# Performance work log

Measured on AMD Instinct MI355X. Metric: run time of the kernel, lower is better.

The kernel has to match this reference:

```python
import jax, jax.numpy as jnp
import numpy as np
import math

D_MODEL = 1024
N_HEADS = 16
B, T = 4, 2048


def setup_inputs() -> dict:
    key = jax.random.key(0)
    ks = jax.random.split(key, 10)
    s = 1.0 / math.sqrt(D_MODEL)
    x = jax.random.normal(ks[0], (B, T, D_MODEL), dtype=jnp.float32)
    # causal mask, broadcastable over batch and heads; 0 -> masked
    mask = jnp.tril(jnp.ones((T, T), dtype=jnp.int32))[None, None, :, :]
    w_q = jax.random.normal(ks[1], (D_MODEL, D_MODEL), dtype=jnp.float32) * s
    b_q = jnp.zeros((D_MODEL,), dtype=jnp.float32)
    w_k = jax.random.normal(ks[2], (D_MODEL, D_MODEL), dtype=jnp.float32) * s
    b_k = jnp.zeros((D_MODEL,), dtype=jnp.float32)
    w_v = jax.random.normal(ks[3], (D_MODEL, D_MODEL), dtype=jnp.float32) * s
    b_v = jnp.zeros((D_MODEL,), dtype=jnp.float32)
    w_o = jax.random.normal(ks[4], (D_MODEL, D_MODEL), dtype=jnp.float32) * s
    b_o = jnp.zeros((D_MODEL,), dtype=jnp.float32)
    return {"x": x, "mask": mask, "w_q": w_q, "b_q": b_q, "w_k": w_k,
            "b_k": b_k, "w_v": w_v, "b_v": b_v, "w_o": w_o, "b_o": b_o}


def reference(x, mask, w_q, b_q, w_k, b_k, w_v, b_v, w_o, b_o):
    Bx, Tx, C = x.shape
    H = N_HEADS
    d_k = C // H
    def split_heads(y):  # [B,T,C] -> [B,H,T,d_k]
        return y.reshape(Bx, Tx, H, d_k).transpose(0, 2, 1, 3)
    Q = split_heads(x @ w_q + b_q)
    K = split_heads(x @ w_k + b_k)
    V = split_heads(x @ w_v + b_v)
    scores = jnp.einsum('bhqd,bhkd->bhqk', Q, K) / math.sqrt(d_k)
    scores = jnp.where(mask == 0, jnp.float32(-1e9), scores)
    attn = jax.nn.softmax(scores, axis=-1)
    out = jnp.einsum('bhqk,bhkd->bhqd', attn, V)
    out = out.transpose(0, 2, 1, 3).reshape(Bx, Tx, C)
    return out @ w_o + b_o
```

## Files before the change

kernel.cpp:

```cpp
#include <hip/hip_runtime.h>
#include <stdint.h>

#define D_MODEL 1024
#define NH      16
#define BB      4
#define TT      2048
#define MROWS   (BB * TT)

typedef __attribute__((ext_vector_type(8))) short bf16x8;
typedef __attribute__((ext_vector_type(4))) float f32x4;

__device__ __forceinline__ unsigned short f2bf(float f) {
    union { float f; unsigned int u; } v; v.f = f;
    unsigned int r = v.u + 0x7fffu + ((v.u >> 16) & 1u);
    return (unsigned short)(r >> 16);
}

__device__ __forceinline__ unsigned short f2bf_fast(float f) {
    union { float f; unsigned int u; } v; v.f = f;
    return (unsigned short)((v.u + 0x8000u) >> 16);
}

__device__ __forceinline__ void gload_lds16(const unsigned short* g, unsigned short* l) {
    __builtin_amdgcn_global_load_lds(
        (const __attribute__((address_space(1))) void*)g,
        (__attribute__((address_space(3))) void*)l,
        16, 0, 0);
}

__global__ void convert_x_kernel(const float* __restrict__ x, unsigned short* __restrict__ xb) {
    int i = blockIdx.x * 256 + threadIdx.x;
    float4 v = ((const float4*)x)[i];
    ushort4 o;
    o.x = f2bf(v.x); o.y = f2bf(v.y); o.z = f2bf(v.z); o.w = f2bf(v.w);
    ((ushort4*)xb)[i] = o;
}

__global__ void transpose_w_kernel(const float* __restrict__ wq, const float* __restrict__ wk,
                                   const float* __restrict__ wv, const float* __restrict__ wo,
                                   unsigned short* tq, unsigned short* tk,
                                   unsigned short* tv, unsigned short* to_) {
    const float* src; unsigned short* dst;
    switch (blockIdx.z) {
        case 0:  src = wq; dst = tq; break;
        case 1:  src = wk; dst = tk; break;
        case 2:  src = wv; dst = tv; break;
        default: src = wo; dst = to_; break;
    }
    __shared__ float tile[32][33];
    int tx = threadIdx.x & 31, ty = threadIdx.x >> 5;
    int k0 = blockIdx.y * 32, n0 = blockIdx.x * 32;
    #pragma unroll
    for (int i = 0; i < 4; ++i)
        tile[ty + i * 8][tx] = src[(k0 + ty + i * 8) * D_MODEL + n0 + tx];
    __syncthreads();
    #pragma unroll
    for (int i = 0; i < 4; ++i)
        dst[(n0 + ty + i * 8) * D_MODEL + k0 + tx] = f2bf(tile[tx][ty + i * 8]);
}

__device__ __forceinline__ void gemm_mainloop(const unsigned short* __restrict__ A,
                                              const unsigned short* __restrict__ Bt,
                                              int m0, int n0,
                                              unsigned short* As, unsigned short* Bs,
                                              f32x4 acc[4][4]) {
    const int tid = threadIdx.x;
    const int lane = tid & 63, wave = tid >> 6;
    const int wm = (wave >> 1) * 64, wn = (wave & 1) * 64;
    const int l15 = lane & 15, quad = lane >> 4;
    const int rx7 = l15 & 7;
    const int srow = tid >> 3;
    const int scol = ((tid & 7) ^ (srow & 7)) * 8;
    const unsigned short* Ag = A + (size_t)(m0 + srow) * D_MODEL + scol;
    const unsigned short* Bg = Bt + (size_t)(n0 + srow) * D_MODEL + scol;
    unsigned short* AsW = As + wave * 512;
    unsigned short* BsW = Bs + wave * 512;
    for (int k0 = 0; k0 < D_MODEL; k0 += 64) {
        __syncthreads();
        #pragma unroll
        for (int p = 0; p < 4; ++p) {
            gload_lds16(Ag + k0 + (size_t)(32 * p) * D_MODEL, AsW + (32 * p) * 64);
            gload_lds16(Bg + k0 + (size_t)(32 * p) * D_MODEL, BsW + (32 * p) * 64);
        }
        __syncthreads();
        #pragma unroll
        for (int kk = 0; kk < 2; ++kk) {
            const int co = ((kk * 4 + quad) ^ rx7) * 8;
            bf16x8 af[4], bfr[4];
            #pragma unroll
            for (int mt = 0; mt < 4; ++mt)
                af[mt] = *(const bf16x8*)(As + (wm + mt * 16 + l15) * 64 + co);
            #pragma unroll
            for (int nt = 0; nt < 4; ++nt)
                bfr[nt] = *(const bf16x8*)(Bs + (wn + nt * 16 + l15) * 64 + co);
            #pragma unroll
            for (int mt = 0; mt < 4; ++mt)
                #pragma unroll
                for (int nt = 0; nt < 4; ++nt)
                    acc[mt][nt] = __builtin_amdgcn_mfma_f32_16x16x32_bf16(af[mt], bfr[nt], acc[mt][nt], 0, 0, 0);
        }
    }
}

__global__ __launch_bounds__(256, 2) void gemm_qkv_kernel(
        const unsigned short* __restrict__ Xb, const unsigned short* __restrict__ Wt,
        const float* __restrict__ bq, const float* __restrict__ bk, const float* __restrict__ bv,
        unsigned short* __restrict__ Qo, unsigned short* __restrict__ Ko,
        unsigned short* __restrict__ VTo) {
    __shared__ unsigned short S[18432];
    unsigned short* As = S;
    unsigned short* Bs = S + 8192;
    int m0 = blockIdx.y * 128, n0 = blockIdx.x * 128;
    f32x4 acc[4][4];
    #pragma unroll
    for (int mt = 0; mt < 4; ++mt)
        #pragma unroll
        for (int nt = 0; nt < 4; ++nt)
            acc[mt][nt] = (f32x4){0.f, 0.f, 0.f, 0.f};
    gemm_mainloop(Xb, Wt, m0, n0, As, Bs, acc);

    const int sel = n0 >> 10;
    const float* bias = (sel == 0) ? bq : (sel == 1) ? bk : bv;
    const float scale = (sel == 0) ? 0.125f * 1.44269504f : 1.f;
    const int tid = threadIdx.x, lane = tid & 63, wave = tid >> 6;
    const int wm = (wave >> 1) * 64, wn = (wave & 1) * 64, l15 = lane & 15, quad = lane >> 4;
    if (sel < 2) {
        unsigned short* Out = (sel == 0) ? Qo : Ko;
        __syncthreads();
        unsigned short* R = S + (wn >> 6) * 9216;
        #pragma unroll
        for (int nt = 0; nt < 4; ++nt) {
            int ln = nt * 16 + l15;
            int col = (n0 + wn + nt * 16 + l15) & 1023;
            float bv_ = bias[col];
            #pragma unroll
            for (int mt = 0; mt < 4; ++mt)
                #pragma unroll
                for (int r = 0; r < 4; ++r) {
                    int lm = wm + mt * 16 + quad * 4 + r;
                    R[lm * 72 + ln] = f2bf((acc[mt][nt][r] + bv_) * scale);
                }
        }
        __syncthreads();
        int hh = tid >> 7, t = tid & 127;
        int h0 = (n0 & 1023) >> 6;
        int b = m0 >> 11, tb = m0 & 2047;
        unsigned short* gp = Out + (size_t)((b * NH + h0 + hh) * TT + tb + t) * 64;
        const unsigned short* lp = S + hh * 9216 + t * 72;
        #pragma unroll
        for (int j = 0; j < 8; ++j)
            *(uint4*)(gp + j * 8) = *(const uint4*)(lp + j * 8);
    } else {
        #pragma unroll
        for (int nt = 0; nt < 4; ++nt) {
            int col = (n0 + wn + nt * 16 + l15) & 1023;
            float bv_ = bias[col];
            int h = col >> 6, dd = col & 63;
            #pragma unroll
            for (int mt = 0; mt < 4; ++mt) {
                int gm0 = m0 + wm + mt * 16 + quad * 4;
                int b = gm0 >> 11, t0 = gm0 & 2047;
                ushort4 o;
                o.x = f2bf(acc[mt][nt][0] + bv_);
                o.y = f2bf(acc[mt][nt][1] + bv_);
                o.z = f2bf(acc[mt][nt][2] + bv_);
                o.w = f2bf(acc[mt][nt][3] + bv_);
                *(ushort4*)&VTo[(((size_t)(b * NH + h) * 16 + (t0 >> 7)) * 64 + dd) * 128 + (t0 & 127)] = o;
            }
        }
    }
}

__global__ __launch_bounds__(256, 2) void gemm_out_kernel(
        const unsigned short* __restrict__ Ob, const unsigned short* __restrict__ Wto,
        const float* __restrict__ bo, float* __restrict__ out) {
    __shared__ unsigned short As[128 * 64], Bs[128 * 64];
    int m0 = blockIdx.y * 128, n0 = blockIdx.x * 128;
    f32x4 acc[4][4];
    #pragma unroll
    for (int mt = 0; mt < 4; ++mt)
        #pragma unroll
        for (int nt = 0; nt < 4; ++nt)
            acc[mt][nt] = (f32x4){0.f, 0.f, 0.f, 0.f};
    gemm_mainloop(Ob, Wto, m0, n0, As, Bs, acc);
    const int tid = threadIdx.x, lane = tid & 63, wave = tid >> 6;
    const int wm = (wave >> 1) * 64, wn = (wave & 1) * 64, l15 = lane & 15, quad = lane >> 4;
    #pragma unroll
    for (int nt = 0; nt < 4; ++nt) {
        int gn = n0 + wn + nt * 16 + l15;
        float bv_ = bo[gn];
        #pragma unroll
        for (int mt = 0; mt < 4; ++mt) {
            #pragma unroll
            for (int r = 0; r < 4; ++r) {
                int gm = m0 + wm + mt * 16 + quad * 4 + r;
                out[(size_t)gm * D_MODEL + gn] = acc[mt][nt][r] + bv_;
            }
        }
    }
}

__global__ __launch_bounds__(256, 2) void flash_kernel(
        const unsigned short* __restrict__ Q, const unsigned short* __restrict__ K,
        const unsigned short* __restrict__ VT, unsigned short* __restrict__ O) {
    __shared__ unsigned short Kd[2][8192];
    __shared__ unsigned short Vd[2][8192];
    __shared__ unsigned short Ps[5120];
    const int n = blockIdx.x;
    const int bh = n & 63;
    const int qt = 15 - (n >> 6);
    const int q0 = qt * 128;
    const int tid = threadIdx.x, lane = tid & 63, wave = tid >> 6;
    const int l15 = lane & 15, quad = lane >> 4;
    const int mbase = wave * 32;
    const unsigned short* Qb = Q + (size_t)bh * (TT * 64) + (size_t)q0 * 64;
    const unsigned short* Kb = K + (size_t)bh * (TT * 64);
    const unsigned short* Vtb = VT + (size_t)bh * (16 * 8192);
    unsigned short* Pw = Ps + wave * 1280;

    int koff[4], voff[4];
    #pragma unroll
    for (int p = 0; p < 4; ++p) {
        int c = p * 256 + wave * 64 + lane;
        int kr = c >> 3, ks = c & 7;
        koff[p] = kr * 64 + ((ks ^ (kr & 7)) * 8);
        int vd = c >> 4, vs = c & 15;
        voff[p] = vd * 128 + ((vs ^ (vd & 15)) * 8);
    }
    auto fire = [&](int kt, int buf) {
        const unsigned short* Ksrc = Kb + kt * 8192;
        const unsigned short* Vsrc = Vtb + kt * 8192;
        #pragma unroll
        for (int p = 0; p < 4; ++p) {
            gload_lds16(Ksrc + koff[p], &Kd[buf][(p * 256 + wave * 64) * 8]);
            gload_lds16(Vsrc + voff[p], &Vd[buf][(p * 256 + wave * 64) * 8]);
        }
    };

    bf16x8 qf[2][2];
    #pragma unroll
    for (int mt = 0; mt < 2; ++mt)
        #pragma unroll
        for (int kk = 0; kk < 2; ++kk)
            qf[mt][kk] = *(const bf16x8*)(Qb + (size_t)(mbase + mt * 16 + l15) * 64 + kk * 32 + quad * 8);

    float l_part[2][4];
    f32x4 acc[2][4];
    #pragma unroll
    for (int mt = 0; mt < 2; ++mt) {
        #pragma unroll
        for (int r = 0; r < 4; ++r) l_part[mt][r] = 0.f;
        #pragma unroll
        for (int nt = 0; nt < 4; ++nt) acc[mt][nt] = (f32x4){0.f, 0.f, 0.f, 0.f};
    }

    fire(0, 0);

    for (int kt = 0; kt <= qt; ++kt) {
        const int p = kt & 1;
        __syncthreads();
        if (kt < qt) fire(kt + 1, p ^ 1);
        const unsigned short* Ksl = Kd[p];
        const unsigned short* Vsl = Vd[p];

        #pragma unroll 1
        for (int s4 = 0; s4 < 4; ++s4) {
            f32x4 sf[2][2];
            #pragma unroll
            for (int mt = 0; mt < 2; ++mt)
                #pragma unroll
                for (int ntl = 0; ntl < 2; ++ntl) sf[mt][ntl] = (f32x4){0.f, 0.f, 0.f, 0.f};
            #pragma unroll
            for (int kk = 0; kk < 2; ++kk)
                #pragma unroll
                for (int ntl = 0; ntl < 2; ++ntl) {
                    int row = s4 * 32 + ntl * 16 + l15;
                    bf16x8 kf = *(const bf16x8*)&Ksl[row * 64 + (((kk * 4 + quad) ^ (row & 7)) * 8)];
                    #pragma unroll
                    for (int mt = 0; mt < 2; ++mt)
                        sf[mt][ntl] = __builtin_amdgcn_mfma_f32_16x16x32_bf16(qf[mt][kk], kf, sf[mt][ntl], 0, 0, 0);
                }
            if (kt == qt) {
                #pragma unroll
                for (int mt = 0; mt < 2; ++mt)
                    #pragma unroll
                    for (int ntl = 0; ntl < 2; ++ntl)
                        #pragma unroll
                        for (int r = 0; r < 4; ++r) {
                            int qi = mbase + mt * 16 + quad * 4 + r;
                            int ki = s4 * 32 + ntl * 16 + l15;
                            if (ki > qi) sf[mt][ntl][r] = -1e30f;
                        }
            }
            #pragma unroll
            for (int mt = 0; mt < 2; ++mt)
                #pragma unroll
                for (int ntl = 0; ntl < 2; ++ntl)
                    #pragma unroll
                    for (int r = 0; r < 4; ++r) {
                        float pv = __builtin_amdgcn_exp2f(sf[mt][ntl][r]);
                        l_part[mt][r] += pv;
                        Pw[(mt * 16 + quad * 4 + r) * 40 + ntl * 16 + l15] = f2bf_fast(pv);
                    }
            bf16x8 pa[2];
            #pragma unroll
            for (int mt = 0; mt < 2; ++mt)
                pa[mt] = *(const bf16x8*)&Pw[(mt * 16 + l15) * 40 + quad * 8];
            #pragma unroll
            for (int ntv = 0; ntv < 4; ++ntv) {
                int d = ntv * 16 + l15;
                bf16x8 vf = *(const bf16x8*)&Vsl[d * 128 + (((s4 * 4 + quad) ^ (d & 15)) * 8)];
                #pragma unroll
                for (int mt = 0; mt < 2; ++mt)
                    acc[mt][ntv] = __builtin_amdgcn_mfma_f32_16x16x32_bf16(pa[mt], vf, acc[mt][ntv], 0, 0, 0);
            }
        }
    }

    const int b = bh >> 4, h = bh & 15;
    float inv[2][4];
    #pragma unroll
    for (int mt = 0; mt < 2; ++mt)
        #pragma unroll
        for (int r = 0; r < 4; ++r) {
            float l = l_part[mt][r];
            l += __shfl_xor(l, 1); l += __shfl_xor(l, 2);
            l += __shfl_xor(l, 4); l += __shfl_xor(l, 8);
            inv[mt][r] = __builtin_amdgcn_rcpf(l);
        }
    __syncthreads();
    unsigned short* Ost = &Kd[0][0];
    #pragma unroll
    for (int mt = 0; mt < 2; ++mt)
        #pragma unroll
        for (int nt = 0; nt < 4; ++nt)
            #pragma unroll
            for (int r = 0; r < 4; ++r)
                Ost[(mbase + mt * 16 + quad * 4 + r) * 72 + nt * 16 + l15] =
                    f2bf(acc[mt][nt][r] * inv[mt][r]);
    __syncthreads();
    {
        int row = tid >> 1, seg = tid & 1;
        unsigned short* gp = O + (size_t)(b * TT + q0 + row) * D_MODEL + h * 64 + seg * 32;
        const unsigned short* lp = Ost + row * 72 + seg * 32;
        #pragma unroll
        for (int j = 0; j < 4; ++j)
            *(uint4*)(gp + j * 8) = *(const uint4*)(lp + j * 8);
    }
}

extern "C" void kernel_launch(void* const* d_in, const int* in_sizes, int n_in,
                              void* d_out, int out_size, void* d_ws, size_t ws_size,
                              hipStream_t stream) {
    const float* x  = (const float*)d_in[0];
    const float* wq = (const float*)d_in[2];
    const float* bq = (const float*)d_in[3];
    const float* wk = (const float*)d_in[4];
    const float* bk = (const float*)d_in[5];
    const float* wv = (const float*)d_in[6];
    const float* bv = (const float*)d_in[7];
    const float* wo = (const float*)d_in[8];
    const float* bo = (const float*)d_in[9];

    char* ws = (char*)d_ws;
    unsigned short* Xb  = (unsigned short*)ws;
    unsigned short* Wtq = (unsigned short*)(ws + (size_t)(16 << 20));
    unsigned short* Wtk = Wtq + (size_t)D_MODEL * D_MODEL;
    unsigned short* Wtv = Wtk + (size_t)D_MODEL * D_MODEL;
    unsigned short* Wto = Wtv + (size_t)D_MODEL * D_MODEL;
    unsigned short* Qb  = Wto + (size_t)D_MODEL * D_MODEL;
    unsigned short* Kb  = Qb + (size_t)MROWS * D_MODEL;
    unsigned short* VTb = Kb + (size_t)MROWS * D_MODEL;
    unsigned short* Ob  = Xb;

    convert_x_kernel<<<(MROWS * D_MODEL) / (256 * 4), 256, 0, stream>>>(x, Xb);
    transpose_w_kernel<<<dim3(32, 32, 4), 256, 0, stream>>>(wq, wk, wv, wo, Wtq, Wtk, Wtv, Wto);
    gemm_qkv_kernel<<<dim3(3 * D_MODEL / 128, MROWS / 128), 256, 0, stream>>>(
        Xb, Wtq, bq, bk, bv, Qb, Kb, VTb);
    flash_kernel<<<dim3(16 * 64), 256, 0, stream>>>(Qb, Kb, VTb, Ob);
    gemm_out_kernel<<<dim3(D_MODEL / 128, MROWS / 128), 256, 0, stream>>>(Ob, Wto, bo, (float*)d_out);
}
```

Measured before the change: 271.1 us.

## Halve flash KV tile to 64 keys, raise occupancy, skip fully-masked wave tiles

Shrinks the per-iteration K/V tile from 128 to 64 keys, which halves LDS usage for the double buffers (about 43KB total) and raises launch bounds to 3 blocks per CU. Iterates twice as many key tiles with a 64-wide V^T swizzle and per-wave early skip of tiles entirely above the causal diagonal. Adds s_setprio around the MFMA sections to favour matrix issue. More barriers per key range and smaller prefetch chunks are the trade-off.

```diff
diff --git a/kernel.cpp b/kernel.cpp
--- a/kernel.cpp
+++ b/kernel.cpp
@@ -200,12 +200,13 @@
     }
 }
 
-__global__ __launch_bounds__(256, 2) void flash_kernel(
+__global__ __launch_bounds__(256, 3) void flash_kernel(
         const unsigned short* __restrict__ Q, const unsigned short* __restrict__ K,
         const unsigned short* __restrict__ VT, unsigned short* __restrict__ O) {
-    __shared__ unsigned short Kd[2][8192];
-    __shared__ unsigned short Vd[2][8192];
-    __shared__ unsigned short Ps[5120];
+    __shared__ unsigned short S[21504];
+    unsigned short* Kd = S;
+    unsigned short* Vd = S + 8192;
+    unsigned short* Ps = S + 16384;
     const int n = blockIdx.x;
     const int bh = n & 63;
     const int qt = 15 - (n >> 6);
@@ -218,22 +219,21 @@
     const unsigned short* Vtb = VT + (size_t)bh * (16 * 8192);
     unsigned short* Pw = Ps + wave * 1280;
 
-    int koff[4], voff[4];
-    #pragma unroll
-    for (int p = 0; p < 4; ++p) {
-        int c = p * 256 + wave * 64 + lane;
-        int kr = c >> 3, ks = c & 7;
-        koff[p] = kr * 64 + ((ks ^ (kr & 7)) * 8);
-        int vd = c >> 4, vs = c & 15;
-        voff[p] = vd * 128 + ((vs ^ (vd & 15)) * 8);
+    int koff[2], voff[2];
+    #pragma unroll
+    for (int p = 0; p < 2; ++p) {
+        int c = p * 256 + tid;
+        int r = c >> 3, s = c & 7;
+        koff[p] = r * 64 + ((s ^ (r & 7)) * 8);
+        voff[p] = r * 128 + ((s ^ (r & 7)) * 8);
     }
     auto fire = [&](int kt, int buf) {
-        const unsigned short* Ksrc = Kb + kt * 8192;
-        const unsigned short* Vsrc = Vtb + kt * 8192;
-        #pragma unroll
-        for (int p = 0; p < 4; ++p) {
-            gload_lds16(Ksrc + koff[p], &Kd[buf][(p * 256 + wave * 64) * 8]);
-            gload_lds16(Vsrc + voff[p], &Vd[buf][(p * 256 + wave * 64) * 8]);
+        const unsigned short* Ksrc = Kb + kt * 4096;
+        const unsigned short* Vsrc = Vtb + (kt >> 1) * 8192 + (kt & 1) * 64;
+        #pragma unroll
+        for (int p = 0; p < 2; ++p) {
+            gload_lds16(Ksrc + koff[p], Kd + buf * 4096 + (p * 256 + wave * 64) * 8);
+            gload_lds16(Vsrc + voff[p], Vd + buf * 4096 + (p * 256 + wave * 64) * 8);
         }
     };
 
@@ -256,20 +256,23 @@
 
     fire(0, 0);
 
-    for (int kt = 0; kt <= qt; ++kt) {
+    const int nkt = 2 * qt + 2;
+    for (int kt = 0; kt < nkt; ++kt) {
         const int p = kt & 1;
         __syncthreads();
-        if (kt < qt) fire(kt + 1, p ^ 1);
-        const unsigned short* Ksl = Kd[p];
-        const unsigned short* Vsl = Vd[p];
+        if (kt + 1 < nkt) fire(kt + 1, p ^ 1);
+        if (kt * 64 > q0 + mbase + 31) continue;
+        const unsigned short* Ksl = Kd + p * 4096;
+        const unsigned short* Vsl = Vd + p * 4096;
 
         #pragma unroll 1
-        for (int s4 = 0; s4 < 4; ++s4) {
+        for (int s4 = 0; s4 < 2; ++s4) {
             f32x4 sf[2][2];
             #pragma unroll
             for (int mt = 0; mt < 2; ++mt)
                 #pragma unroll
                 for (int ntl = 0; ntl < 2; ++ntl) sf[mt][ntl] = (f32x4){0.f, 0.f, 0.f, 0.f};
+            __builtin_amdgcn_s_setprio(1);
             #pragma unroll
             for (int kk = 0; kk < 2; ++kk)
                 #pragma unroll
@@ -280,7 +283,9 @@
                     for (int mt = 0; mt < 2; ++mt)
                         sf[mt][ntl] = __builtin_amdgcn_mfma_f32_16x16x32_bf16(qf[mt][kk], kf, sf[mt][ntl], 0, 0, 0);
                 }
-            if (kt == qt) {
+            __builtin_amdgcn_s_setprio(0);
+            if (kt >= 2 * qt) {
+                const int kofs = (kt - 2 * qt) * 64;
                 #pragma unroll
                 for (int mt = 0; mt < 2; ++mt)
                     #pragma unroll
@@ -288,7 +293,7 @@
                         #pragma unroll
                         for (int r = 0; r < 4; ++r) {
                             int qi = mbase + mt * 16 + quad * 4 + r;
-                            int ki = s4 * 32 + ntl * 16 + l15;
+                            int ki = kofs + s4 * 32 + ntl * 16 + l15;
                             if (ki > qi) sf[mt][ntl][r] = -1e30f;
                         }
             }
@@ -306,14 +311,16 @@
             #pragma unroll
             for (int mt = 0; mt < 2; ++mt)
                 pa[mt] = *(const bf16x8*)&Pw[(mt * 16 + l15) * 40 + quad * 8];
+            __builtin_amdgcn_s_setprio(1);
             #pragma unroll
             for (int ntv = 0; ntv < 4; ++ntv) {
                 int d = ntv * 16 + l15;
-                bf16x8 vf = *(const bf16x8*)&Vsl[d * 128 + (((s4 * 4 + quad) ^ (d & 15)) * 8)];
+                bf16x8 vf = *(const bf16x8*)&Vsl[d * 64 + (((s4 * 4 + quad) ^ (d & 7)) * 8)];
                 #pragma unroll
                 for (int mt = 0; mt < 2; ++mt)
                     acc[mt][ntv] = __builtin_amdgcn_mfma_f32_16x16x32_bf16(pa[mt], vf, acc[mt][ntv], 0, 0, 0);
             }
+            __builtin_amdgcn_s_setprio(0);
         }
     }
 
@@ -329,7 +336,7 @@
             inv[mt][r] = __builtin_amdgcn_rcpf(l);
         }
     __syncthreads();
-    unsigned short* Ost = &Kd[0][0];
+    unsigned short* Ost = S;
     #pragma unroll
     for (int mt = 0; mt < 2; ++mt)
         #pragma unroll
```

After: 263.9 us. 2.6% less time.
